# Performance work log

Measured on AMD Instinct MI355X. Metric: run time of the kernel, lower is better.

The kernel has to match this reference:

```python
import jax, jax.numpy as jnp
import numpy as np

N_HEADS = 16
NEG_FILL = -1000000000.0  # masked_fill value from the torch module
PADDING = 0.0             # default padding arg


def setup_inputs() -> dict:
    key = jax.random.key(0)
    kq, kk, kv = jax.random.split(key, 3)
    B, S, D = 2, 2048, 1024
    q = jax.random.normal(kq, (B, S, D), dtype=jnp.float32)
    k = jax.random.normal(kk, (B, S, D), dtype=jnp.float32)
    v = jax.random.normal(kv, (B, S, D), dtype=jnp.float32)
    return {"q": q, "k": k, "v": v, "is_masked": 1}


def reference(q, k, v, is_masked):
    B, S, D = q.shape
    d_key = D // N_HEADS

    def split_heads(x):  # [B,S,D] -> [B,H,S,d_key]
        return x.reshape(B, S, N_HEADS, d_key).transpose(0, 2, 1, 3)

    qh, kh, vh = split_heads(q), split_heads(k), split_heads(v)
    scale = 1.0 / jnp.sqrt(jnp.asarray(d_key, dtype=q.dtype))
    # [B,H,S,S] raw attention scores
    scores = jnp.einsum("bhqd,bhkd->bhqk", qh, kh) * scale
    # value-based mask: keep positions where score != padding
    mask = scores != PADDING
    if is_masked:
        causal = jnp.tril(jnp.ones((S, S), dtype=bool))  # [S,S]
        mask = mask & causal
    scores = jnp.where(mask, scores, jnp.asarray(NEG_FILL, dtype=scores.dtype))
    probs = jax.nn.softmax(scores, axis=-1)
    out = jnp.einsum("bhqk,bhkd->bhqd", probs, vh)  # [B,H,S,d_key]
    return out.transpose(0, 2, 1, 3).reshape(B, S, D)
```

## Files before the change

### kernel.cpp

```cpp
#include <hip/hip_runtime.h>
#include <hip/hip_bf16.h>
#include <math.h>

typedef __bf16   bf16x8 __attribute__((ext_vector_type(8)));
typedef _Float16 f16x4  __attribute__((ext_vector_type(4)));
typedef float    f32x4  __attribute__((ext_vector_type(4)));

#define S_LEN 2048
#define D_MODEL 1024
#define LT 72
#define CEXP 0.18033688011112042f

__device__ __forceinline__ float fast_exp2(float x) {
    return __builtin_amdgcn_exp2f(x);
}

template<bool BF>
__device__ __forceinline__ void body(
    const void* __restrict__ qv, const void* __restrict__ kv,
    const void* __restrict__ vv, void* __restrict__ outv,
    int maskflag, int z, int bh,
    __bf16* Ks0, __bf16* Ks1, _Float16* Vt0, _Float16* Vt1)
{
    const int b    = bh >> 4;
    const int h    = bh & 15;
    const int t    = threadIdx.x;
    const int w    = t >> 6;
    const int lane = t & 63;
    const int m16  = lane & 15;
    const int quad = lane >> 4;

    const int qtA = z, qtB = 31 - z;
    const int q0A = qtA * 64, q0B = qtB * 64;

    const size_t head_off = (size_t)b * S_LEN * D_MODEL + (size_t)h * 64;

    const __bf16* qb = (const __bf16*)qv; const float* qf = (const float*)qv;
    const __bf16* kb = (const __bf16*)kv; const float* kf = (const float*)kv;
    const __bf16* vb = (const __bf16*)vv; const float* vf = (const float*)vv;

    bf16x8 aqA0, aqA1, aqB0, aqB1;
    {
        const int rA = q0A + w * 16 + m16, rB = q0B + w * 16 + m16;
        if (BF) {
            const __bf16* pA = qb + head_off + (size_t)rA * D_MODEL;
            const __bf16* pB = qb + head_off + (size_t)rB * D_MODEL;
            aqA0 = *(const bf16x8*)&pA[quad * 8];
            aqA1 = *(const bf16x8*)&pA[32 + quad * 8];
            aqB0 = *(const bf16x8*)&pB[quad * 8];
            aqB1 = *(const bf16x8*)&pB[32 + quad * 8];
            #pragma unroll
            for (int j = 0; j < 8; ++j) {
                aqA0[j] = (__bf16)((float)aqA0[j] * CEXP);
                aqA1[j] = (__bf16)((float)aqA1[j] * CEXP);
                aqB0[j] = (__bf16)((float)aqB0[j] * CEXP);
                aqB1[j] = (__bf16)((float)aqB1[j] * CEXP);
            }
        } else {
            const float* pA = qf + head_off + (size_t)rA * D_MODEL;
            const float* pB = qf + head_off + (size_t)rB * D_MODEL;
            #pragma unroll
            for (int half = 0; half < 2; ++half) {
                float4 x0 = *(const float4*)&pA[half * 32 + quad * 8];
                float4 x1 = *(const float4*)&pA[half * 32 + quad * 8 + 4];
                float4 y0 = *(const float4*)&pB[half * 32 + quad * 8];
                float4 y1 = *(const float4*)&pB[half * 32 + quad * 8 + 4];
                bf16x8 fa = { (__bf16)(x0.x*CEXP), (__bf16)(x0.y*CEXP),
                              (__bf16)(x0.z*CEXP), (__bf16)(x0.w*CEXP),
                              (__bf16)(x1.x*CEXP), (__bf16)(x1.y*CEXP),
                              (__bf16)(x1.z*CEXP), (__bf16)(x1.w*CEXP) };
                bf16x8 fb = { (__bf16)(y0.x*CEXP), (__bf16)(y0.y*CEXP),
                              (__bf16)(y0.z*CEXP), (__bf16)(y0.w*CEXP),
                              (__bf16)(y1.x*CEXP), (__bf16)(y1.y*CEXP),
                              (__bf16)(y1.z*CEXP), (__bf16)(y1.w*CEXP) };
                if (half == 0) { aqA0 = fa; aqB0 = fb; } else { aqA1 = fa; aqB1 = fb; }
            }
        }
    }

    f32x4 oA[4], oB[4];
    #pragma unroll
    for (int i = 0; i < 4; ++i) { oA[i] = (f32x4){0.f,0.f,0.f,0.f}; oB[i] = oA[i]; }
    float lsumA = 0.f, lsumB = 0.f;

    const int kg = t >> 4, dg = t & 15;
    const int k0 = kg * 4, d0 = dg * 4;
    const int cst = k0 ^ ((dg & 7) << 3);

    const int ktmax = maskflag ? qtB : (S_LEN / 64 - 1);

    float4 kr[4], vr[4];
    auto pref = [&](int kt) {
        if (BF) {
            const __bf16* base = kb + head_off + (size_t)kt * 64 * D_MODEL;
            #pragma unroll
            for (int i = 0; i < 2; ++i) {
                int c = t + i * 256, row = c >> 3, off = (c & 7) << 3;
                *(uint4*)&kr[i] = *(const uint4*)&base[(size_t)row * D_MODEL + off];
            }
            const __bf16* vp = vb + head_off + (size_t)(kt * 64 + k0) * D_MODEL + d0;
            #pragma unroll
            for (int j = 0; j < 4; ++j)
                *(uint2*)&vr[j] = *(const uint2*)&vp[(size_t)j * D_MODEL];
        } else {
            const float* base = kf + head_off + (size_t)kt * 64 * D_MODEL;
            #pragma unroll
            for (int i = 0; i < 4; ++i) {
                int c = t + i * 256, row = c >> 4, off = (c & 15) << 2;
                kr[i] = *(const float4*)&base[(size_t)row * D_MODEL + off];
            }
            const float* vp = vf + head_off + (size_t)(kt * 64 + k0) * D_MODEL + d0;
            #pragma unroll
            for (int j = 0; j < 4; ++j)
                vr[j] = *(const float4*)&vp[(size_t)j * D_MODEL];
        }
    };
    auto stage = [&](__bf16* Ks, _Float16* Vt) {
        if (BF) {
            #pragma unroll
            for (int i = 0; i < 2; ++i) {
                int c = t + i * 256, row = c >> 3, off = (c & 7) << 3;
                *(uint4*)&Ks[row * LT + off] = *(const uint4*)&kr[i];
            }
            union { uint2 u; __bf16 hh[4]; } r[4];
            #pragma unroll
            for (int j = 0; j < 4; ++j) r[j].u = *(const uint2*)&vr[j];
            #pragma unroll
            for (int j = 0; j < 4; ++j) {
                _Float16 pk[4] = { (_Float16)(float)r[0].hh[j], (_Float16)(float)r[1].hh[j],
                                   (_Float16)(float)r[2].hh[j], (_Float16)(float)r[3].hh[j] };
                *(uint2*)&Vt[(d0 + j) * LT + cst] = *(uint2*)pk;
            }
        } else {
            #pragma unroll
            for (int i = 0; i < 4; ++i) {
                int c = t + i * 256, row = c >> 4, off = (c & 15) << 2;
                float4 ld = kr[i];
                __bf16 pk[4] = { (__bf16)ld.x, (__bf16)ld.y, (__bf16)ld.z, (__bf16)ld.w };
                *(uint2*)&Ks[row * LT + off] = *(uint2*)pk;
            }
            #pragma unroll
            for (int j = 0; j < 4; ++j) {
                _Float16 pk[4] = { (_Float16)vr[0][j], (_Float16)vr[1][j],
                                   (_Float16)vr[2][j], (_Float16)vr[3][j] };
                *(uint2*)&Vt[(d0 + j) * LT + cst] = *(uint2*)pk;
            }
        }
    };

    const int qloc = w * 16 + m16;

    pref(0);
    for (int kt = 0; kt <= ktmax; ++kt) {
        __bf16*   Ks = (kt & 1) ? Ks1 : Ks0;
        _Float16* Vt = (kt & 1) ? Vt1 : Vt0;
        stage(Ks, Vt);
        __syncthreads();
        if (kt < ktmax) pref(kt + 1);

        const bool activeA = (!maskflag) || (kt <= qtA);
        const bool diagA = maskflag && (kt == qtA);
        const bool diagB = maskflag && (kt == qtB);

        f32x4 sA[4], sB[4];
        #pragma unroll
        for (int nt = 0; nt < 4; ++nt) {
            bf16x8 bk0 = *(bf16x8*)&Ks[(nt * 16 + m16) * LT + quad * 8];
            bf16x8 bk1 = *(bf16x8*)&Ks[(nt * 16 + m16) * LT + 32 + quad * 8];
            f32x4 acc = (f32x4){0.f,0.f,0.f,0.f};
            acc = __builtin_amdgcn_mfma_f32_16x16x32_bf16(bk0, aqB0, acc, 0, 0, 0);
            acc = __builtin_amdgcn_mfma_f32_16x16x32_bf16(bk1, aqB1, acc, 0, 0, 0);
            sB[nt] = acc;
            if (activeA) {
                f32x4 acc2 = (f32x4){0.f,0.f,0.f,0.f};
                acc2 = __builtin_amdgcn_mfma_f32_16x16x32_bf16(bk0, aqA0, acc2, 0, 0, 0);
                acc2 = __builtin_amdgcn_mfma_f32_16x16x32_bf16(bk1, aqA1, acc2, 0, 0, 0);
                sA[nt] = acc2;
            }
        }

        #pragma unroll
        for (int g = 0; g < 4; ++g) {
            f16x4 bv[4];
            #pragma unroll
            for (int dt = 0; dt < 4; ++dt) {
                const int dim = dt * 16 + m16;
                const int sw = ((dim >> 2) & 7) << 3;
                bv[dt] = *(f16x4*)&Vt[dim * LT + ((g * 16 + quad * 4) ^ sw)];
            }
            {
                f16x4 ap;
                #pragma unroll
                for (int reg = 0; reg < 4; ++reg) {
                    float raw = sB[g][reg];
                    float p = fast_exp2(raw);
                    if (diagB) {
                        bool valid = (raw != 0.0f) && ((g * 16 + quad * 4 + reg) <= qloc);
                        p = valid ? p : 0.0f;
                    }
                    lsumB += p;
                    ap[reg] = (_Float16)p;
                }
                #pragma unroll
                for (int dt = 0; dt < 4; ++dt)
                    oB[dt] = __builtin_amdgcn_mfma_f32_16x16x16f16(ap, bv[dt], oB[dt], 0, 0, 0);
            }
            if (activeA) {
                f16x4 ap;
                #pragma unroll
                for (int reg = 0; reg < 4; ++reg) {
                    float raw = sA[g][reg];
                    float p = fast_exp2(raw);
                    if (diagA) {
                        bool valid = (raw != 0.0f) && ((g * 16 + quad * 4 + reg) <= qloc);
                        p = valid ? p : 0.0f;
                    }
                    lsumA += p;
                    ap[reg] = (_Float16)p;
                }
                #pragma unroll
                for (int dt = 0; dt < 4; ++dt)
                    oA[dt] = __builtin_amdgcn_mfma_f32_16x16x16f16(ap, bv[dt], oA[dt], 0, 0, 0);
            }
        }
    }

    auto epilogue = [&](f32x4* o, float lsum, int q0) {
        float l = lsum;
        l += __shfl_xor(l, 16, 64);
        l += __shfl_xor(l, 32, 64);
        #pragma unroll
        for (int reg = 0; reg < 4; ++reg) {
            float li = __shfl(l, quad * 4 + reg, 64);
            float invl = 1.0f / li;
            int srow = q0 + w * 16 + quad * 4 + reg;
            #pragma unroll
            for (int dt = 0; dt < 4; ++dt) {
                size_t idx = head_off + (size_t)srow * D_MODEL + dt * 16 + m16;
                float val = o[dt][reg] * invl;
                if (BF) ((__bf16*)outv)[idx] = (__bf16)val;
                else    ((float*)outv)[idx]  = val;
            }
        }
    };
    epilogue(oB, lsumB, q0B);
    epilogue(oA, lsumA, q0A);
}

__global__ __launch_bounds__(256, 2)
void mha_flash_kernel(const void* __restrict__ qv,
                      const void* __restrict__ kv,
                      const void* __restrict__ vv,
                      const int* __restrict__ is_masked_p,
                      void* __restrict__ outv)
{
    __shared__ __attribute__((aligned(16))) __bf16   Ks0[64 * LT];
    __shared__ __attribute__((aligned(16))) __bf16   Ks1[64 * LT];
    __shared__ __attribute__((aligned(16))) _Float16 Vt0[64 * LT];
    __shared__ __attribute__((aligned(16))) _Float16 Vt1[64 * LT];

    const int id  = blockIdx.x;
    const int xcd = id & 7;
    const int r   = id >> 3;
    const int bh  = xcd * 4 + (r & 3);
    const int z   = r >> 2;

    const int maskflag = *is_masked_p;

    const __bf16* qprobe = (const __bf16*)qv;
    float px = (float)qprobe[2 * (threadIdx.x & 63)];
    bool okp = (px == px) && (fabsf(px) > 1e-6f) && (fabsf(px) < 100.0f);
    unsigned long long bal = __ballot(okp);
    const bool isbf16 = (__popcll(bal) >= 48);

    if (isbf16)
        body<true >(qv, kv, vv, outv, maskflag, z, bh, Ks0, Ks1, Vt0, Vt1);
    else
        body<false>(qv, kv, vv, outv, maskflag, z, bh, Ks0, Ks1, Vt0, Vt1);
}

extern "C" void kernel_launch(void* const* d_in, const int* in_sizes, int n_in,
                              void* d_out, int out_size, void* d_ws, size_t ws_size,
                              hipStream_t stream) {
    const int* is_masked = (const int*)d_in[3];
    mha_flash_kernel<<<dim3(512), 256, 0, stream>>>(d_in[0], d_in[1], d_in[2], is_masked, d_out);
}
```

Measured before the change: 129.1 us.

## Split key range across two blocks per query tile and combine via workspace

Each (head, query-tile pair) is now handled by two blocks that process alternating (even/odd) key tiles, doubling the grid and raising launch bounds occupancy to 4 blocks per CU. The odd block publishes its partial output and row sums to a workspace with release stores. The even block spin-waits on those flags, merges the partials and normalises. This aims to expose more parallelism and shorten the per-block causal loop. In exchange it adds extra global traffic and a cross-block spin dependency that needs both blocks co-resident. It also relies on workspace flags that are never reset between calls, so stale flags from a previous call could be read.

```diff
diff --git a/kernel.cpp b/kernel.cpp
--- a/kernel.cpp
+++ b/kernel.cpp
@@ -15,11 +15,12 @@
     return __builtin_amdgcn_exp2f(x);
 }
 
+
 template<bool BF>
 __device__ __forceinline__ void body(
     const void* __restrict__ qv, const void* __restrict__ kv,
-    const void* __restrict__ vv, void* __restrict__ outv,
-    int maskflag, int z, int bh,
+    const void* __restrict__ vv, void* __restrict__ outv, void* __restrict__ wsv,
+    int maskflag, int z, int bh, int par,
     __bf16* Ks0, __bf16* Ks1, _Float16* Vt0, _Float16* Vt1)
 {
     const int b    = bh >> 4;
@@ -38,6 +39,10 @@
     const __bf16* qb = (const __bf16*)qv; const float* qf = (const float*)qv;
     const __bf16* kb = (const __bf16*)kv; const float* kf = (const float*)kv;
     const __bf16* vb = (const __bf16*)vv; const float* vf = (const float*)vv;
+
+    float* lws = (float*)wsv;
+    float* pOf = BF ? (float*)((char*)wsv + (1 << 20))
+                    : (float*)outv;
 
     bf16x8 aqA0, aqA1, aqB0, aqB1;
     {
@@ -87,7 +92,8 @@
     const int k0 = kg * 4, d0 = dg * 4;
     const int cst = k0 ^ ((dg & 7) << 3);
 
-    const int ktmax = maskflag ? qtB : (S_LEN / 64 - 1);
+    const int LB = maskflag ? qtB : 31;
+    const int LA = maskflag ? qtA : 31;
 
     float4 kr[4], vr[4];
     auto pref = [&](int kt) {
@@ -150,15 +156,16 @@
 
     const int qloc = w * 16 + m16;
 
-    pref(0);
-    for (int kt = 0; kt <= ktmax; ++kt) {
-        __bf16*   Ks = (kt & 1) ? Ks1 : Ks0;
-        _Float16* Vt = (kt & 1) ? Vt1 : Vt0;
+    pref(par);
+    int i = 0;
+    for (int kt = par; kt <= LB; kt += 2, ++i) {
+        __bf16*   Ks = (i & 1) ? Ks1 : Ks0;
+        _Float16* Vt = (i & 1) ? Vt1 : Vt0;
         stage(Ks, Vt);
         __syncthreads();
-        if (kt < ktmax) pref(kt + 1);
-
-        const bool activeA = (!maskflag) || (kt <= qtA);
+        if (kt + 2 <= LB) pref(kt + 2);
+
+        const bool activeA = (!maskflag) || (kt <= LA);
         const bool diagA = maskflag && (kt == qtA);
         const bool diagB = maskflag && (kt == qtB);
 
@@ -225,34 +232,81 @@
         }
     }
 
-    auto epilogue = [&](f32x4* o, float lsum, int q0) {
-        float l = lsum;
-        l += __shfl_xor(l, 16, 64);
-        l += __shfl_xor(l, 32, 64);
-        #pragma unroll
-        for (int reg = 0; reg < 4; ++reg) {
-            float li = __shfl(l, quad * 4 + reg, 64);
-            float invl = 1.0f / li;
-            int srow = q0 + w * 16 + quad * 4 + reg;
-            #pragma unroll
-            for (int dt = 0; dt < 4; ++dt) {
-                size_t idx = head_off + (size_t)srow * D_MODEL + dt * 16 + m16;
-                float val = o[dt][reg] * invl;
-                if (BF) ((__bf16*)outv)[idx] = (__bf16)val;
-                else    ((float*)outv)[idx]  = val;
-            }
-        }
-    };
-    epilogue(oB, lsumB, q0B);
-    epilogue(oA, lsumA, q0A);
+    float lB = lsumB;
+    lB += __shfl_xor(lB, 16, 64);
+    lB += __shfl_xor(lB, 32, 64);
+    float lA = lsumA;
+    lA += __shfl_xor(lA, 16, 64);
+    lA += __shfl_xor(lA, 32, 64);
+
+    const int lbase = bh * S_LEN;
+
+    if (par == 1) {
+        auto publish = [&](f32x4* o, int q0) {
+            #pragma unroll
+            for (int reg = 0; reg < 4; ++reg) {
+                int srow = q0 + w * 16 + quad * 4 + reg;
+                #pragma unroll
+                for (int dt = 0; dt < 4; ++dt) {
+                    size_t idx = head_off + (size_t)srow * D_MODEL + dt * 16 + m16;
+                    __hip_atomic_store(&pOf[idx], o[dt][reg],
+                                       __ATOMIC_RELAXED, __HIP_MEMORY_SCOPE_AGENT);
+                }
+            }
+        };
+        publish(oB, q0B);
+        publish(oA, q0A);
+        if (quad == 0) {
+            __hip_atomic_store(&lws[lbase + q0B + w * 16 + m16], lB + 1.0f,
+                               __ATOMIC_RELEASE, __HIP_MEMORY_SCOPE_AGENT);
+            __hip_atomic_store(&lws[lbase + q0A + w * 16 + m16], lA + 1.0f,
+                               __ATOMIC_RELEASE, __HIP_MEMORY_SCOPE_AGENT);
+        }
+    } else {
+        auto combine = [&](f32x4* o, float lown, int q0) {
+            float lp[4];
+            #pragma unroll
+            for (int reg = 0; reg < 4; ++reg) {
+                int srow = q0 + w * 16 + quad * 4 + reg;
+                float lv = __hip_atomic_load(&lws[lbase + srow],
+                                             __ATOMIC_ACQUIRE, __HIP_MEMORY_SCOPE_AGENT);
+                int guard = 0;
+                while (lv < 0.5f && guard < (1 << 25)) {
+                    __builtin_amdgcn_s_sleep(1);
+                    lv = __hip_atomic_load(&lws[lbase + srow],
+                                           __ATOMIC_ACQUIRE, __HIP_MEMORY_SCOPE_AGENT);
+                    ++guard;
+                }
+                lp[reg] = lv - 1.0f;
+            }
+            #pragma unroll
+            for (int reg = 0; reg < 4; ++reg) {
+                float li = __shfl(lown, quad * 4 + reg, 64);
+                float invl = 1.0f / (li + lp[reg]);
+                int srow = q0 + w * 16 + quad * 4 + reg;
+                #pragma unroll
+                for (int dt = 0; dt < 4; ++dt) {
+                    size_t idx = head_off + (size_t)srow * D_MODEL + dt * 16 + m16;
+                    float pv = __hip_atomic_load(&pOf[idx],
+                                                 __ATOMIC_RELAXED, __HIP_MEMORY_SCOPE_AGENT);
+                    float val = (o[dt][reg] + pv) * invl;
+                    if (BF) ((__bf16*)outv)[idx] = (__bf16)val;
+                    else    ((float*)outv)[idx]  = val;
+                }
+            }
+        };
+        combine(oB, lB, q0B);
+        combine(oA, lA, q0A);
+    }
 }
 
-__global__ __launch_bounds__(256, 2)
+__global__ __launch_bounds__(256, 4)
 void mha_flash_kernel(const void* __restrict__ qv,
                       const void* __restrict__ kv,
                       const void* __restrict__ vv,
                       const int* __restrict__ is_masked_p,
-                      void* __restrict__ outv)
+                      void* __restrict__ outv,
+                      void* __restrict__ wsv)
 {
     __shared__ __attribute__((aligned(16))) __bf16   Ks0[64 * LT];
     __shared__ __attribute__((aligned(16))) __bf16   Ks1[64 * LT];
@@ -262,8 +316,9 @@
     const int id  = blockIdx.x;
     const int xcd = id & 7;
     const int r   = id >> 3;
-    const int bh  = xcd * 4 + (r & 3);
-    const int z   = r >> 2;
+    const int par = r & 1;
+    const int bh  = xcd * 4 + ((r >> 1) & 3);
+    const int z   = r >> 3;
 
     const int maskflag = *is_masked_p;
 
@@ -274,14 +329,15 @@
     const bool isbf16 = (__popcll(bal) >= 48);
 
     if (isbf16)
-        body<true >(qv, kv, vv, outv, maskflag, z, bh, Ks0, Ks1, Vt0, Vt1);
+        body<true >(qv, kv, vv, outv, wsv, maskflag, z, bh, par, Ks0, Ks1, Vt0, Vt1);
     else
-        body<false>(qv, kv, vv, outv, maskflag, z, bh, Ks0, Ks1, Vt0, Vt1);
+        body<false>(qv, kv, vv, outv, wsv, maskflag, z, bh, par, Ks0, Ks1, Vt0, Vt1);
 }
 
 extern "C" void kernel_launch(void* const* d_in, const int* in_sizes, int n_in,
                               void* d_out, int out_size, void* d_ws, size_t ws_size,
                               hipStream_t stream) {
     const int* is_masked = (const int*)d_in[3];
-    mha_flash_kernel<<<dim3(512), 256, 0, stream>>>(d_in[0], d_in[1], d_in[2], is_masked, d_out);
+    mha_flash_kernel<<<dim3(1024), 256, 0, stream>>>(d_in[0], d_in[1], d_in[2],
+                                                     is_masked, d_out, d_ws);
 }
```

New measurement: 446.3 us. 3.46x slower.

## Split key tiles across two thread groups per block and combine partial outputs

Applied to the files above, without the earlier changes.

Each block now runs 512 threads split into two 256-thread groups. One group processes even key tiles and the other odd key tiles, each with its own double-buffered K/V shared memory. The partial outputs and row sums are then combined through shared memory before the normalized output is written. This doubles the parallelism available per query tile so the long causal loop runs in about half the iterations. In exchange it doubles shared memory per block, adds a reduction step, and changes launch bounds to 512 threads at 4 waves/SIMD, which may constrain registers.

```diff
diff --git a/kernel.cpp b/kernel.cpp
--- a/kernel.cpp
+++ b/kernel.cpp
@@ -15,18 +15,19 @@
     return __builtin_amdgcn_exp2f(x);
 }
 
+
 template<bool BF>
 __device__ __forceinline__ void body(
     const void* __restrict__ qv, const void* __restrict__ kv,
     const void* __restrict__ vv, void* __restrict__ outv,
-    int maskflag, int z, int bh,
-    __bf16* Ks0, __bf16* Ks1, _Float16* Vt0, _Float16* Vt1)
+    int maskflag, int z, int bh, int par,
+    __bf16* Ks0, __bf16* Ks1, _Float16* Vt0, _Float16* Vt1, float* comb)
 {
     const int b    = bh >> 4;
     const int h    = bh & 15;
-    const int t    = threadIdx.x;
-    const int w    = t >> 6;
-    const int lane = t & 63;
+    const int t8   = threadIdx.x & 255;
+    const int w    = t8 >> 6;
+    const int lane = threadIdx.x & 63;
     const int m16  = lane & 15;
     const int quad = lane >> 4;
 
@@ -83,11 +84,12 @@
     for (int i = 0; i < 4; ++i) { oA[i] = (f32x4){0.f,0.f,0.f,0.f}; oB[i] = oA[i]; }
     float lsumA = 0.f, lsumB = 0.f;
 
-    const int kg = t >> 4, dg = t & 15;
+    const int kg = t8 >> 4, dg = t8 & 15;
     const int k0 = kg * 4, d0 = dg * 4;
     const int cst = k0 ^ ((dg & 7) << 3);
 
-    const int ktmax = maskflag ? qtB : (S_LEN / 64 - 1);
+    const int LB  = maskflag ? qtB : (S_LEN / 64 - 1);
+    const int NIT = (LB >> 1) + 1;
 
     float4 kr[4], vr[4];
     auto pref = [&](int kt) {
@@ -95,7 +97,7 @@
             const __bf16* base = kb + head_off + (size_t)kt * 64 * D_MODEL;
             #pragma unroll
             for (int i = 0; i < 2; ++i) {
-                int c = t + i * 256, row = c >> 3, off = (c & 7) << 3;
+                int c = t8 + i * 256, row = c >> 3, off = (c & 7) << 3;
                 *(uint4*)&kr[i] = *(const uint4*)&base[(size_t)row * D_MODEL + off];
             }
             const __bf16* vp = vb + head_off + (size_t)(kt * 64 + k0) * D_MODEL + d0;
@@ -106,7 +108,7 @@
             const float* base = kf + head_off + (size_t)kt * 64 * D_MODEL;
             #pragma unroll
             for (int i = 0; i < 4; ++i) {
-                int c = t + i * 256, row = c >> 4, off = (c & 15) << 2;
+                int c = t8 + i * 256, row = c >> 4, off = (c & 15) << 2;
                 kr[i] = *(const float4*)&base[(size_t)row * D_MODEL + off];
             }
             const float* vp = vf + head_off + (size_t)(kt * 64 + k0) * D_MODEL + d0;
@@ -119,7 +121,7 @@
         if (BF) {
             #pragma unroll
             for (int i = 0; i < 2; ++i) {
-                int c = t + i * 256, row = c >> 3, off = (c & 7) << 3;
+                int c = t8 + i * 256, row = c >> 3, off = (c & 7) << 3;
                 *(uint4*)&Ks[row * LT + off] = *(const uint4*)&kr[i];
             }
             union { uint2 u; __bf16 hh[4]; } r[4];
@@ -134,7 +136,7 @@
         } else {
             #pragma unroll
             for (int i = 0; i < 4; ++i) {
-                int c = t + i * 256, row = c >> 4, off = (c & 15) << 2;
+                int c = t8 + i * 256, row = c >> 4, off = (c & 15) << 2;
                 float4 ld = kr[i];
                 __bf16 pk[4] = { (__bf16)ld.x, (__bf16)ld.y, (__bf16)ld.z, (__bf16)ld.w };
                 *(uint2*)&Ks[row * LT + off] = *(uint2*)pk;
@@ -150,13 +152,16 @@
 
     const int qloc = w * 16 + m16;
 
-    pref(0);
-    for (int kt = 0; kt <= ktmax; ++kt) {
-        __bf16*   Ks = (kt & 1) ? Ks1 : Ks0;
-        _Float16* Vt = (kt & 1) ? Vt1 : Vt0;
-        stage(Ks, Vt);
+    pref(par);
+    for (int i = 0; i < NIT; ++i) {
+        const int kt = 2 * i + par;
+        const bool act = (kt <= LB);
+        __bf16*   Ks = (i & 1) ? Ks1 : Ks0;
+        _Float16* Vt = (i & 1) ? Vt1 : Vt0;
+        if (act) stage(Ks, Vt);
         __syncthreads();
-        if (kt < ktmax) pref(kt + 1);
+        if (kt + 2 <= LB) pref(kt + 2);
+        if (!act) continue;
 
         const bool activeA = (!maskflag) || (kt <= qtA);
         const bool diagA = maskflag && (kt == qtA);
@@ -225,39 +230,64 @@
         }
     }
 
-    auto epilogue = [&](f32x4* o, float lsum, int q0) {
-        float l = lsum;
-        l += __shfl_xor(l, 16, 64);
-        l += __shfl_xor(l, 32, 64);
+    float lB = lsumB;
+    lB += __shfl_xor(lB, 16, 64);
+    lB += __shfl_xor(lB, 32, 64);
+    float lA = lsumA;
+    lA += __shfl_xor(lA, 16, 64);
+    lA += __shfl_xor(lA, 32, 64);
+
+    __syncthreads();
+    if (par == 1) {
+        float* c = comb + t8 * 36;
         #pragma unroll
-        for (int reg = 0; reg < 4; ++reg) {
-            float li = __shfl(l, quad * 4 + reg, 64);
-            float invl = 1.0f / li;
-            int srow = q0 + w * 16 + quad * 4 + reg;
-            #pragma unroll
-            for (int dt = 0; dt < 4; ++dt) {
-                size_t idx = head_off + (size_t)srow * D_MODEL + dt * 16 + m16;
-                float val = o[dt][reg] * invl;
-                if (BF) ((__bf16*)outv)[idx] = (__bf16)val;
-                else    ((float*)outv)[idx]  = val;
-            }
-        }
-    };
-    epilogue(oB, lsumB, q0B);
-    epilogue(oA, lsumA, q0A);
+        for (int dt = 0; dt < 4; ++dt) {
+            *(f32x4*)(c + dt * 4)      = oB[dt];
+            *(f32x4*)(c + 16 + dt * 4) = oA[dt];
+        }
+        c[32] = lB;
+        c[33] = lA;
+    }
+    __syncthreads();
+    if (par == 0) {
+        const float* c = comb + t8 * 36;
+        #pragma unroll
+        for (int dt = 0; dt < 4; ++dt) {
+            oB[dt] += *(const f32x4*)(c + dt * 4);
+            oA[dt] += *(const f32x4*)(c + 16 + dt * 4);
+        }
+        lB += c[32];
+        lA += c[33];
+
+        auto epilogue = [&](f32x4* o, float lsum, int q0) {
+            #pragma unroll
+            for (int reg = 0; reg < 4; ++reg) {
+                float li = __shfl(lsum, quad * 4 + reg, 64);
+                float invl = 1.0f / li;
+                int srow = q0 + w * 16 + quad * 4 + reg;
+                #pragma unroll
+                for (int dt = 0; dt < 4; ++dt) {
+                    size_t idx = head_off + (size_t)srow * D_MODEL + dt * 16 + m16;
+                    float val = o[dt][reg] * invl;
+                    if (BF) ((__bf16*)outv)[idx] = (__bf16)val;
+                    else    ((float*)outv)[idx]  = val;
+                }
+            }
+        };
+        epilogue(oB, lB, q0B);
+        epilogue(oA, lA, q0A);
+    }
 }
 
-__global__ __launch_bounds__(256, 2)
+__global__ __launch_bounds__(512, 4)
 void mha_flash_kernel(const void* __restrict__ qv,
                       const void* __restrict__ kv,
                       const void* __restrict__ vv,
                       const int* __restrict__ is_masked_p,
                       void* __restrict__ outv)
 {
-    __shared__ __attribute__((aligned(16))) __bf16   Ks0[64 * LT];
-    __shared__ __attribute__((aligned(16))) __bf16   Ks1[64 * LT];
-    __shared__ __attribute__((aligned(16))) _Float16 Vt0[64 * LT];
-    __shared__ __attribute__((aligned(16))) _Float16 Vt1[64 * LT];
+    __shared__ __attribute__((aligned(16))) __bf16   KsBuf[2][2][64 * LT];
+    __shared__ __attribute__((aligned(16))) _Float16 VtBuf[2][2][64 * LT];
 
     const int id  = blockIdx.x;
     const int xcd = id & 7;
@@ -265,6 +295,7 @@
     const int bh  = xcd * 4 + (r & 3);
     const int z   = r >> 2;
 
+    const int par = (threadIdx.x >> 8) & 1;
     const int maskflag = *is_masked_p;
 
     const __bf16* qprobe = (const __bf16*)qv;
@@ -273,15 +304,22 @@
     unsigned long long bal = __ballot(okp);
     const bool isbf16 = (__popcll(bal) >= 48);
 
+    float* comb = (float*)&KsBuf[0][0][0];
+
     if (isbf16)
-        body<true >(qv, kv, vv, outv, maskflag, z, bh, Ks0, Ks1, Vt0, Vt1);
+        body<true >(qv, kv, vv, outv, maskflag, z, bh, par,
+                    &KsBuf[par][0][0], &KsBuf[par][1][0],
+                    &VtBuf[par][0][0], &VtBuf[par][1][0], comb);
     else
-        body<false>(qv, kv, vv, outv, maskflag, z, bh, Ks0, Ks1, Vt0, Vt1);
+        body<false>(qv, kv, vv, outv, maskflag, z, bh, par,
+                    &KsBuf[par][0][0], &KsBuf[par][1][0],
+                    &VtBuf[par][0][0], &VtBuf[par][1][0], comb);
 }
 
 extern "C" void kernel_launch(void* const* d_in, const int* in_sizes, int n_in,
                               void* d_out, int out_size, void* d_ws, size_t ws_size,
                               hipStream_t stream) {
     const int* is_masked = (const int*)d_in[3];
-    mha_flash_kernel<<<dim3(512), 256, 0, stream>>>(d_in[0], d_in[1], d_in[2], is_masked, d_out);
+    mha_flash_kernel<<<dim3(512), 512, 0, stream>>>(d_in[0], d_in[1], d_in[2],
+                                                    is_masked, d_out);
 }
```

After: 224.1 us. 1.74x slower.
